# Kernel optimization log

Hardware: AMD Instinct MI355X
Metric: run time of the kernel (lower is better)

Reference implementation:

```python
import jax, jax.numpy as jnp
import numpy as np

# dims: batch, dna_seq_len, protein_emb, decoder_size, ffn hidden, vocab, layers, heads
B, T, P, D, F, V, L, H = 64, 128, 1024, 512, 2048, 4096, 4, 8


def _sinusoid_pe(T, D):
    pos = np.arange(T, dtype=np.float32)[:, None]
    div = np.exp(np.arange(0, D, 2, dtype=np.float32) * (-np.log(10000.0) / D))
    pe = np.zeros((T, D), dtype=np.float32)
    pe[:, 0::2] = np.sin(pos * div)
    pe[:, 1::2] = np.cos(pos * div)
    return jnp.asarray(pe)


def setup_inputs() -> dict:
    key = jax.random.key(0)
    ks = iter(jax.random.split(key, 24))
    n = lambda *shape: jax.random.normal(next(ks), shape, jnp.float32) * 0.02
    return dict(
        protein_embeddings=jax.random.normal(next(ks), (B, P), jnp.float32),
        input_token=jax.random.randint(next(ks), (B,), 0, V),
        proj1_w=n(P, 2 * D), proj1_b=jnp.zeros((2 * D,), jnp.float32),
        proj2_w=n(2 * D, D), proj2_b=jnp.zeros((D,), jnp.float32),
        emb=n(V, D),
        sa_w=n(L, 4, D, D), sa_b=jnp.zeros((L, 4, D), jnp.float32),
        ca_w=n(L, 4, D, D), ca_b=jnp.zeros((L, 4, D), jnp.float32),
        ffn_w1=n(L, D, F), ffn_b1=jnp.zeros((L, F), jnp.float32),
        ffn_w2=n(L, F, D), ffn_b2=jnp.zeros((L, D), jnp.float32),
        ln_g=jnp.ones((L, 3, D), jnp.float32), ln_b=jnp.zeros((L, 3, D), jnp.float32),
        out_w=n(D, V), out_b=jnp.zeros((V,), jnp.float32),
        pe=_sinusoid_pe(T, D),
    )


def _layer_norm(x, g, b, eps=1e-5):
    m = jnp.mean(x, -1, keepdims=True)
    v = jnp.var(x, -1, keepdims=True)
    return (x - m) * jax.lax.rsqrt(v + eps) * g + b


def _forward(protein_embeddings, input_token, proj1_w, proj1_b, proj2_w, proj2_b,
             emb, sa_w, sa_b, ca_w, ca_b, ffn_w1, ffn_b1, ffn_w2, ffn_b2,
             ln_g, ln_b, out_w, out_b, pe):
    dh = D // H
    scale = 1.0 / jnp.sqrt(jnp.float32(dh))
    # protein -> decoder memory: Linear(P, 2D) -> ReLU -> Linear(2D, D),
    # then repeated along seq dim (memory rows are all identical).
    h = jax.nn.relu(protein_embeddings @ proj1_w + proj1_b)
    mem1 = h @ proj2_w + proj2_b                         # [B, D]
    mem = jnp.broadcast_to(mem1[:, None, :], (B, T, D))  # [B, T, D]
    # Cross-attn K/V are constant across decode steps: precompute per layer.
    K = (jnp.einsum('btd,lde->lbte', mem, ca_w[:, 1]) + ca_b[:, 1][:, None, None, :]).reshape(L, B, T, H, dh)
    Vv = (jnp.einsum('btd,lde->lbte', mem, ca_w[:, 2]) + ca_b[:, 2][:, None, None, :]).reshape(L, B, T, H, dh)

    def step(token, t):
        # query length == 1 (the module embeds only the current token each step)
        x = emb[token] + pe[t]                           # [B, D]
        for l in range(L):
            # self-attn over a single key: softmax over one score == 1,
            # so attn output reduces to Wo(Wv x + bv) + bo
            sa = (x @ sa_w[l, 2] + sa_b[l, 2]) @ sa_w[l, 3] + sa_b[l, 3]
            x = _layer_norm(x + sa, ln_g[l, 0], ln_b[l, 0])
            # cross-attention over protein memory
            q = ((x @ ca_w[l, 0] + ca_b[l, 0]) * scale).reshape(B, H, dh)
            s = jnp.einsum('bhe,bthe->bht', q, K[l])
            a = jax.nn.softmax(s, -1)
            o = jnp.einsum('bht,bthe->bhe', a, Vv[l]).reshape(B, D)
            ca = o @ ca_w[l, 3] + ca_b[l, 3]
            x = _layer_norm(x + ca, ln_g[l, 1], ln_b[l, 1])
            # FFN (ReLU, post-LN as in PyTorch default TransformerDecoderLayer)
            f = jax.nn.relu(x @ ffn_w1[l] + ffn_b1[l]) @ ffn_w2[l] + ffn_b2[l]
            x = _layer_norm(x + f, ln_g[l, 2], ln_b[l, 2])
        logits = x @ out_w + out_b                       # [B, V]
        probs = jax.nn.softmax(logits, -1)
        return jnp.argmax(probs, -1), probs

    _, probs_t = jax.lax.scan(step, input_token, jnp.arange(T))
    return jnp.transpose(probs_t, (1, 0, 2))             # [B, T, V]


def reference(protein_embeddings, input_token, proj1_w, proj1_b, proj2_w, proj2_b,
              emb, sa_w, sa_b, ca_w, ca_b, ffn_w1, ffn_b1, ffn_w2, ffn_b2,
              ln_g, ln_b, out_w, out_b, pe):
    return _forward(protein_embeddings, input_token, proj1_w, proj1_b, proj2_w, proj2_b,
                    emb, sa_w, sa_b, ca_w, ca_b, ffn_w1, ffn_b1, ffn_w2, ffn_b2,
                    ln_g, ln_b, out_w, out_b, pe)
```

## Files before the change

### kernel.cpp

```cpp
#include <hip/hip_runtime.h>


#define B 64
#define T 128
#define PP 1024
#define D 512
#define F 2048
#define V 4096
#define XP 20

typedef const float* fp;

static __device__ __forceinline__ float wred(float s){
    #pragma unroll
    for (int o = 32; o > 0; o >>= 1) s += __shfl_xor(s, o, 64);
    return s;
}

__global__ __launch_bounds__(256) void k_setup_mem(
    fp prot, fp p1w, fp p1b, fp p2w, fp p2b,
    fp caw, fp cab, float* ca_out)
{
    __shared__ float xp[PP];
    __shared__ float hr[PP];
    __shared__ float m1[D];
    __shared__ float tv[D];
    int b = blockIdx.x, tid = threadIdx.x;
    for (int i = tid; i < PP; i += 256) xp[i] = prot[b*PP + i];
    __syncthreads();
    for (int c = tid; c < 1024; c += 256){
        float acc = p1b[c];
        for (int k = 0; k < PP; k++) acc = fmaf(xp[k], p1w[k*1024 + c], acc);
        hr[c] = fmaxf(acc, 0.f);
    }
    __syncthreads();
    for (int c = tid; c < D; c += 256){
        float acc = p2b[c];
        for (int k = 0; k < 1024; k++) acc = fmaf(hr[k], p2w[k*D + c], acc);
        m1[c] = acc;
    }
    __syncthreads();
    for (int l = 0; l < 4; l++){
        const float* wv = caw + (size_t)(l*4 + 2)*D*D;
        const float* bv = cab + (l*4 + 2)*D;
        for (int c = tid; c < D; c += 256){
            float acc = bv[c];
            for (int k = 0; k < D; k++) acc = fmaf(m1[k], wv[k*D + c], acc);
            tv[c] = acc;
        }
        __syncthreads();
        const float* wo = caw + (size_t)(l*4 + 3)*D*D;
        const float* bo = cab + (l*4 + 3)*D;
        for (int c = tid; c < D; c += 256){
            float acc = bo[c];
            for (int k = 0; k < D; k++) acc = fmaf(tv[k], wo[k*D + c], acc);
            ca_out[(l*B + b)*D + c] = acc;
        }
        __syncthreads();
    }
}

__global__ __launch_bounds__(256) void k_fold_sa(
    fp saw, fp sab, float* wfold, float* bfold)
{
    int l = blockIdx.x >> 6;
    int kb = blockIdx.x & 63;
    int tid = threadIdx.x;
    const float* Wv = saw + (size_t)(l*4 + 2)*D*D;
    const float* Wo = saw + (size_t)(l*4 + 3)*D*D;
    __shared__ float a[8][D];
    for (int i = tid; i < 8*D; i += 256){
        int r = i >> 9, m = i & 511;
        a[r][m] = Wv[(kb*8 + r)*D + m];
    }
    __syncthreads();
    for (int cc = 0; cc < 2; cc++){
        int c = tid + cc*256;
        float acc[8];
        #pragma unroll
        for (int r = 0; r < 8; r++) acc[r] = 0.f;
        for (int m = 0; m < D; m++){
            float w = Wo[m*D + c];
            #pragma unroll
            for (int r = 0; r < 8; r++) acc[r] = fmaf(a[r][m], w, acc[r]);
        }
        #pragma unroll
        for (int r = 0; r < 8; r++){
            int kg = kb*8 + r;
            wfold[((size_t)l*D + kg)*D + c] = acc[r] + (kg == c ? 1.f : 0.f);
        }
    }
    if (kb == 0){
        const float* bv = sab + (l*4 + 2)*D;
        const float* bo = sab + (l*4 + 3)*D;
        for (int c = tid; c < D; c += 256){
            float acc = bo[c];
            for (int m = 0; m < D; m++) acc = fmaf(bv[m], Wo[m*D + c], acc);
            bfold[l*D + c] = acc;
        }
    }
}


static __device__ void pro_emb(float* xt, const int* tok, fp emb, fp pe,
                               int t, int r0, int d0, int tid)
{
    int lane = tid & 63, wid = tid >> 6;
    for (int i = 0; i < 4; i++){
        int rr = wid*4 + i;
        int tk = tok[r0 + rr];
        const float* er = emb + (size_t)tk*D + d0;
        const float* pr = pe + t*D + d0;
        #pragma unroll
        for (int j = 0; j < 4; j++){
            int d = lane + j*64;
            xt[d*XP + rr] = er[d] + pr[d];
        }
    }
}

static __device__ void pro_ln4(float* xt, const float* u3, fp g, fp bb,
                               int r0, int d0, int tid)
{
    int lane = tid & 63, wid = tid >> 6;
    int jb = d0 >> 6;
    for (int i = 0; i < 4; i++){
        int rr = wid*4 + i, r = r0 + rr;
        float e[8]; float s = 0.f, sq = 0.f;
        #pragma unroll
        for (int j = 0; j < 8; j++){
            int d = lane + j*64;
            float v = u3[r*D + d] + u3[B*D + r*D + d]
                    + u3[2*B*D + r*D + d] + u3[3*B*D + r*D + d];
            e[j] = v; s += v; sq += v*v;
        }
        s = wred(s); sq = wred(sq);
        float mu = s*(1.f/D);
        float rs = rsqrtf(sq*(1.f/D) - mu*mu + 1e-5f);
        #pragma unroll
        for (int j = 0; j < 8; j++){
            int d = lane + j*64;
            if (j >= jb && j < jb + 4)
                xt[(d - d0)*XP + rr] = (e[j]-mu)*rs*g[d] + bb[d];
        }
    }
}

static __device__ void pro_ln2(float* xt, float* zc, const float* u1, const float* ca,
                               fp g0, fp b0, fp g1, fp b1,
                               int r0, int d0, int c0, int tid)
{
    int lane = tid & 63, wid = tid >> 6;
    int jb = d0 >> 6, jc = c0 >> 6;
    for (int i = 0; i < 4; i++){
        int rr = wid*4 + i, r = r0 + rr;
        float e[8]; float s = 0.f, sq = 0.f;
        #pragma unroll
        for (int j = 0; j < 8; j++){
            int d = lane + j*64;
            float v = u1[r*D + d] + u1[B*D + r*D + d];
            e[j] = v; s += v; sq += v*v;
        }
        s = wred(s); sq = wred(sq);
        float mu = s*(1.f/D), rs = rsqrtf(sq*(1.f/D) - mu*mu + 1e-5f);
        s = 0.f; sq = 0.f;
        #pragma unroll
        for (int j = 0; j < 8; j++){
            int d = lane + j*64;
            float v = (e[j]-mu)*rs*g0[d] + b0[d] + ca[r*D + d];
            e[j] = v; s += v; sq += v*v;
        }
        s = wred(s); sq = wred(sq);
        mu = s*(1.f/D); rs = rsqrtf(sq*(1.f/D) - mu*mu + 1e-5f);
        #pragma unroll
        for (int j = 0; j < 8; j++){
            int d = lane + j*64;
            float z = (e[j]-mu)*rs*g1[d] + b1[d];
            if (xt && j >= jb && j < jb + 4) xt[(d - d0)*XP + rr] = z;
            if (zc && j == jc) zc[rr*64 + lane] = z;
        }
    }
}


__global__ __launch_bounds__(256) void k_sa(
    const float* wfold, const float* bfold, const float* u3,
    fp lng, fp lnb, const int* tok, fp emb, fp pe,
    float* u1, int l, int t)
{
    __shared__ float xt[256*XP];
    int bx = blockIdx.x;
    int cb = bx & 7, rbg = (bx >> 3) & 3, ks = bx >> 5;
    int tid = threadIdx.x;
    int r0 = rbg*16, d0 = ks*256;
    if (l == 0) pro_emb(xt, tok, emb, pe, t, r0, d0, tid);
    else        pro_ln4(xt, u3, lng + ((l-1)*3+2)*D, lnb + ((l-1)*3+2)*D, r0, d0, tid);
    __syncthreads();
    int lane = tid & 63, rb = tid >> 6;
    int c = cb*64 + lane;
    const float* W = wfold + (size_t)l*D*D + (size_t)d0*D + c;
    float bias = (ks == 0) ? bfold[l*D + c] : 0.f;
    float a0=bias, a1=bias, a2=bias, a3=bias;
    const float* xc = xt + rb*4;
    #pragma unroll 8
    for (int k = 0; k < 256; k++){
        float w = W[(size_t)k*D];
        float4 xv = *(const float4*)(xc + k*XP);
        a0 = fmaf(xv.x, w, a0); a1 = fmaf(xv.y, w, a1);
        a2 = fmaf(xv.z, w, a2); a3 = fmaf(xv.w, w, a3);
    }
    int r = r0 + rb*4;
    float* o = u1 + ks*B*D;
    o[(r+0)*D + c] = a0; o[(r+1)*D + c] = a1;
    o[(r+2)*D + c] = a2; o[(r+3)*D + c] = a3;
}

__global__ __launch_bounds__(256) void k_ffn1(
    const float* u1, const float* ca, fp lng, fp lnb,
    fp w1, fp b1, float* h, int l)
{
    __shared__ float zt[256*XP];
    int bx = blockIdx.x;
    int cb = bx & 31, rbg = (bx >> 5) & 3, ks = bx >> 7;
    int tid = threadIdx.x;
    int r0 = rbg*16, d0 = ks*256;
    pro_ln2(zt, nullptr, u1, ca + l*B*D,
            lng + l*3*D, lnb + l*3*D, lng + (l*3+1)*D, lnb + (l*3+1)*D,
            r0, d0, 0, tid);
    __syncthreads();
    int lane = tid & 63, rb = tid >> 6;
    int c = cb*64 + lane;
    const float* W = w1 + (size_t)l*D*F + (size_t)d0*F + c;
    float bias = (ks == 0) ? b1[l*F + c] : 0.f;
    float a0=bias, a1=bias, a2=bias, a3=bias;
    const float* xc = zt + rb*4;
    #pragma unroll 8
    for (int k = 0; k < 256; k++){
        float w = W[(size_t)k*F];
        float4 xv = *(const float4*)(xc + k*XP);
        a0 = fmaf(xv.x, w, a0); a1 = fmaf(xv.y, w, a1);
        a2 = fmaf(xv.z, w, a2); a3 = fmaf(xv.w, w, a3);
    }
    int r = r0 + rb*4;
    float* o = h + ks*B*F;
    o[(r+0)*F + c] = a0; o[(r+1)*F + c] = a1;
    o[(r+2)*F + c] = a2; o[(r+3)*F + c] = a3;
}

__global__ __launch_bounds__(256) void k_ffn2(
    const float* u1, const float* ca, fp lng, fp lnb,
    const float* h, fp w2, fp b2, float* u3, int l)
{
    __shared__ float ht[512*XP];
    __shared__ float zc[16*64];
    int bx = blockIdx.x;
    int cb = bx & 7, rbg = (bx >> 3) & 3, kh = bx >> 5;
    int tid = threadIdx.x;
    int r0 = rbg*16, c0 = cb*64;
    if (kh == 0)
        pro_ln2(nullptr, zc, u1, ca + l*B*D,
                lng + l*3*D, lnb + l*3*D, lng + (l*3+1)*D, lnb + (l*3+1)*D,
                r0, 0, c0, tid);
    for (int i = tid; i < 16*512; i += 256){
        int rr = i >> 9, kk = i & 511;
        int gi = (r0+rr)*F + kh*512 + kk;
        ht[kk*XP + rr] = fmaxf(h[gi] + h[B*F + gi], 0.f);
    }
    __syncthreads();
    int lane = tid & 63, rb = tid >> 6;
    int c = c0 + lane;
    const float* W = w2 + (size_t)l*F*D + (size_t)kh*512*D + c;
    float a0, a1, a2, a3;
    if (kh == 0){
        float bb = b2[l*D + c];
        a0 = bb + zc[(rb*4+0)*64 + lane];
        a1 = bb + zc[(rb*4+1)*64 + lane];
        a2 = bb + zc[(rb*4+2)*64 + lane];
        a3 = bb + zc[(rb*4+3)*64 + lane];
    } else { a0=a1=a2=a3=0.f; }
    const float* xc = ht + rb*4;
    #pragma unroll 8
    for (int k = 0; k < 512; k++){
        float w = W[(size_t)k*D];
        float4 xv = *(const float4*)(xc + k*XP);
        a0 = fmaf(xv.x, w, a0); a1 = fmaf(xv.y, w, a1);
        a2 = fmaf(xv.z, w, a2); a3 = fmaf(xv.w, w, a3);
    }
    int r = r0 + rb*4;
    float* o = u3 + kh*B*D;
    o[(r+0)*D + c] = a0; o[(r+1)*D + c] = a1;
    o[(r+2)*D + c] = a2; o[(r+3)*D + c] = a3;
}

__global__ __launch_bounds__(256) void k_logits(
    const float* u3, fp lng, fp lnb, fp outw, fp outb, float* lgt)
{
    __shared__ float xt[256*XP];
    int bx = blockIdx.x;
    int cb = bx & 63, rbg = (bx >> 6) & 3, ks = bx >> 8;
    int tid = threadIdx.x;
    int r0 = rbg*16, d0 = ks*256;
    pro_ln4(xt, u3, lng + 11*D, lnb + 11*D, r0, d0, tid);
    __syncthreads();
    int lane = tid & 63, rb = tid >> 6;
    int c = cb*64 + lane;
    const float* W = outw + (size_t)d0*V + c;
    float bias = (ks == 0) ? outb[c] : 0.f;
    float a0=bias, a1=bias, a2=bias, a3=bias;
    const float* xc = xt + rb*4;
    #pragma unroll 8
    for (int k = 0; k < 256; k++){
        float w = W[(size_t)k*V];
        float4 xv = *(const float4*)(xc + k*XP);
        a0 = fmaf(xv.x, w, a0); a1 = fmaf(xv.y, w, a1);
        a2 = fmaf(xv.z, w, a2); a3 = fmaf(xv.w, w, a3);
    }
    int r = r0 + rb*4;
    float* o = lgt + ks*B*V;
    o[(r+0)*V + c] = a0; o[(r+1)*V + c] = a1;
    o[(r+2)*V + c] = a2; o[(r+3)*V + c] = a3;
}

__global__ __launch_bounds__(256) void k_final(
    const float* lgt, float* out, int* tok, int t)
{
    int b = blockIdx.x, tid = threadIdx.x;
    int lane = tid & 63, wid = tid >> 6;
    __shared__ float sm[4]; __shared__ int si[4]; __shared__ float ss[4];
    const float* l0 = lgt + b*V;
    const float* l1 = lgt + B*V + b*V;
    float m = -3.4e38f; int mi = 0;
    for (int i = tid; i < V; i += 256){
        float v = l0[i] + l1[i];
        if (v > m){ m = v; mi = i; }
    }
    #pragma unroll
    for (int o = 32; o > 0; o >>= 1){
        float om = __shfl_xor(m, o, 64);
        int   oi = __shfl_xor(mi, o, 64);
        if (om > m || (om == m && oi < mi)){ m = om; mi = oi; }
    }
    if (lane == 0){ sm[wid] = m; si[wid] = mi; }
    __syncthreads();
    if (tid == 0){
        #pragma unroll
        for (int w = 1; w < 4; w++)
            if (sm[w] > sm[0] || (sm[w] == sm[0] && si[w] < si[0])){ sm[0]=sm[w]; si[0]=si[w]; }
        tok[b] = si[0];
    }
    __syncthreads();
    m = sm[0];
    float s = 0.f;
    for (int i = tid; i < V; i += 256) s += expf(l0[i] + l1[i] - m);
    s = wred(s);
    if (lane == 0) ss[wid] = s;
    __syncthreads();
    float inv = 1.f / (ss[0] + ss[1] + ss[2] + ss[3]);
    float* orow = out + ((size_t)b*T + t)*V;
    for (int i = tid; i < V; i += 256)
        orow[i] = expf(l0[i] + l1[i] - m) * inv;
}

extern "C" void kernel_launch(void* const* d_in, const int* in_sizes, int n_in,
                              void* d_out, int out_size, void* d_ws, size_t ws_size,
                              hipStream_t stream)
{
    fp prot = (fp)d_in[0];
    const int* itok = (const int*)d_in[1];
    fp p1w=(fp)d_in[2], p1b=(fp)d_in[3], p2w=(fp)d_in[4], p2b=(fp)d_in[5];
    fp emb=(fp)d_in[6], saw=(fp)d_in[7], sab=(fp)d_in[8];
    fp caw=(fp)d_in[9], cab=(fp)d_in[10];
    fp w1=(fp)d_in[11], b1=(fp)d_in[12], w2=(fp)d_in[13], b2=(fp)d_in[14];
    fp lng=(fp)d_in[15], lnb=(fp)d_in[16];
    fp outw=(fp)d_in[17], outb=(fp)d_in[18], pe=(fp)d_in[19];

    char* w = (char*)d_ws;
    float* wfold = (float*)w;  w += (size_t)4*D*D*4;
    float* bfold = (float*)w;  w += 4*D*4;
    float* ca_o  = (float*)w;  w += 4*B*D*4;
    float* u1    = (float*)w;  w += 2*B*D*4;
    float* hbuf  = (float*)w;  w += 2*B*F*4;
    float* u3    = (float*)w;  w += 4*B*D*4;
    float* lgt   = (float*)w;  w += 2*B*V*4;
    int*   tok   = (int*)w;    w += 256;

    float* out = (float*)d_out;

    k_setup_mem<<<64, 256, 0, stream>>>(prot, p1w, p1b, p2w, p2b, caw, cab, ca_o);
    k_fold_sa<<<256, 256, 0, stream>>>(saw, sab, wfold, bfold);

    for (int t = 0; t < T; t++){
        const int* tsrc = (t == 0) ? itok : tok;
        for (int l = 0; l < 4; l++){
            k_sa  <<<64,  256, 0, stream>>>(wfold, bfold, u3, lng, lnb, tsrc, emb, pe, u1, l, t);
            k_ffn1<<<256, 256, 0, stream>>>(u1, ca_o, lng, lnb, w1, b1, hbuf, l);
            k_ffn2<<<128, 256, 0, stream>>>(u1, ca_o, lng, lnb, hbuf, w2, b2, u3, l);
        }
        k_logits<<<512, 256, 0, stream>>>(u3, lng, lnb, outw, outb, lgt);
        k_final <<<64,  256, 0, stream>>>(lgt, out, tok, t);
    }
}
```

Before: 45.07 ms.

## Replace per-step kernel launches with one persistent per-row decode kernel

Replaces the 1,800 small per-step, per-layer kernel launches with a single persistent kernel. It launches one 1024-thread block per batch row, and that block runs all 128 decode steps, the 4 layers, the logits and the softmax/argmax in shared memory. This removes launch overhead and global round-trips of intermediates. In exchange, each of the 64 blocks streams every weight matrix independently from L2/HBM every step, so weight reuse across batch rows is lost. Only 64 CUs are used.

New measurement: 85.22 ms. +89.1%, slower.

```diff
diff --git a/kernel.cpp b/kernel.cpp
--- a/kernel.cpp
+++ b/kernel.cpp
@@ -7,7 +7,6 @@
 #define D 512
 #define F 2048
 #define V 4096
-#define XP 20
 
 typedef const float* fp;
 
@@ -101,264 +100,183 @@
     }
 }
 
-
-static __device__ void pro_emb(float* xt, const int* tok, fp emb, fp pe,
-                               int t, int r0, int d0, int tid)
+__global__ __launch_bounds__(1024) void k_row_decode(
+    const float* wfold, const float* bfold, const float* ca_o,
+    fp lng, fp lnb, const int* itok, fp emb, fp pe,
+    fp w1, fp b1, fp w2, fp b2, fp outw, fp outb, float* out)
 {
-    int lane = tid & 63, wid = tid >> 6;
-    for (int i = 0; i < 4; i++){
-        int rr = wid*4 + i;
-        int tk = tok[r0 + rr];
-        const float* er = emb + (size_t)tk*D + d0;
-        const float* pr = pe + t*D + d0;
-        #pragma unroll
-        for (int j = 0; j < 4; j++){
-            int d = lane + j*64;
-            xt[d*XP + rr] = er[d] + pr[d];
-        }
-    }
-}
-
-static __device__ void pro_ln4(float* xt, const float* u3, fp g, fp bb,
-                               int r0, int d0, int tid)
-{
-    int lane = tid & 63, wid = tid >> 6;
-    int jb = d0 >> 6;
-    for (int i = 0; i < 4; i++){
-        int rr = wid*4 + i, r = r0 + rr;
-        float e[8]; float s = 0.f, sq = 0.f;
-        #pragma unroll
-        for (int j = 0; j < 8; j++){
-            int d = lane + j*64;
-            float v = u3[r*D + d] + u3[B*D + r*D + d]
-                    + u3[2*B*D + r*D + d] + u3[3*B*D + r*D + d];
-            e[j] = v; s += v; sq += v*v;
-        }
-        s = wred(s); sq = wred(sq);
-        float mu = s*(1.f/D);
-        float rs = rsqrtf(sq*(1.f/D) - mu*mu + 1e-5f);
-        #pragma unroll
-        for (int j = 0; j < 8; j++){
-            int d = lane + j*64;
-            if (j >= jb && j < jb + 4)
-                xt[(d - d0)*XP + rr] = (e[j]-mu)*rs*g[d] + bb[d];
-        }
-    }
-}
-
-static __device__ void pro_ln2(float* xt, float* zc, const float* u1, const float* ca,
-                               fp g0, fp b0, fp g1, fp b1,
-                               int r0, int d0, int c0, int tid)
-{
-    int lane = tid & 63, wid = tid >> 6;
-    int jb = d0 >> 6, jc = c0 >> 6;
-    for (int i = 0; i < 4; i++){
-        int rr = wid*4 + i, r = r0 + rr;
-        float e[8]; float s = 0.f, sq = 0.f;
-        #pragma unroll
-        for (int j = 0; j < 8; j++){
-            int d = lane + j*64;
-            float v = u1[r*D + d] + u1[B*D + r*D + d];
-            e[j] = v; s += v; sq += v*v;
-        }
-        s = wred(s); sq = wred(sq);
-        float mu = s*(1.f/D), rs = rsqrtf(sq*(1.f/D) - mu*mu + 1e-5f);
-        s = 0.f; sq = 0.f;
-        #pragma unroll
-        for (int j = 0; j < 8; j++){
-            int d = lane + j*64;
-            float v = (e[j]-mu)*rs*g0[d] + b0[d] + ca[r*D + d];
-            e[j] = v; s += v; sq += v*v;
-        }
-        s = wred(s); sq = wred(sq);
-        mu = s*(1.f/D); rs = rsqrtf(sq*(1.f/D) - mu*mu + 1e-5f);
-        #pragma unroll
-        for (int j = 0; j < 8; j++){
-            int d = lane + j*64;
-            float z = (e[j]-mu)*rs*g1[d] + b1[d];
-            if (xt && j >= jb && j < jb + 4) xt[(d - d0)*XP + rr] = z;
-            if (zc && j == jc) zc[rr*64 + lane] = z;
-        }
-    }
-}
-
-
-__global__ __launch_bounds__(256) void k_sa(
-    const float* wfold, const float* bfold, const float* u3,
-    fp lng, fp lnb, const int* tok, fp emb, fp pe,
-    float* u1, int l, int t)
-{
-    __shared__ float xt[256*XP];
-    int bx = blockIdx.x;
-    int cb = bx & 7, rbg = (bx >> 3) & 3, ks = bx >> 5;
-    int tid = threadIdx.x;
-    int r0 = rbg*16, d0 = ks*256;
-    if (l == 0) pro_emb(xt, tok, emb, pe, t, r0, d0, tid);
-    else        pro_ln4(xt, u3, lng + ((l-1)*3+2)*D, lnb + ((l-1)*3+2)*D, r0, d0, tid);
-    __syncthreads();
-    int lane = tid & 63, rb = tid >> 6;
-    int c = cb*64 + lane;
-    const float* W = wfold + (size_t)l*D*D + (size_t)d0*D + c;
-    float bias = (ks == 0) ? bfold[l*D + c] : 0.f;
-    float a0=bias, a1=bias, a2=bias, a3=bias;
-    const float* xc = xt + rb*4;
-    #pragma unroll 8
-    for (int k = 0; k < 256; k++){
-        float w = W[(size_t)k*D];
-        float4 xv = *(const float4*)(xc + k*XP);
-        a0 = fmaf(xv.x, w, a0); a1 = fmaf(xv.y, w, a1);
-        a2 = fmaf(xv.z, w, a2); a3 = fmaf(xv.w, w, a3);
-    }
-    int r = r0 + rb*4;
-    float* o = u1 + ks*B*D;
-    o[(r+0)*D + c] = a0; o[(r+1)*D + c] = a1;
-    o[(r+2)*D + c] = a2; o[(r+3)*D + c] = a3;
-}
-
-__global__ __launch_bounds__(256) void k_ffn1(
-    const float* u1, const float* ca, fp lng, fp lnb,
-    fp w1, fp b1, float* h, int l)
-{
-    __shared__ float zt[256*XP];
-    int bx = blockIdx.x;
-    int cb = bx & 31, rbg = (bx >> 5) & 3, ks = bx >> 7;
-    int tid = threadIdx.x;
-    int r0 = rbg*16, d0 = ks*256;
-    pro_ln2(zt, nullptr, u1, ca + l*B*D,
-            lng + l*3*D, lnb + l*3*D, lng + (l*3+1)*D, lnb + (l*3+1)*D,
-            r0, d0, 0, tid);
-    __syncthreads();
-    int lane = tid & 63, rb = tid >> 6;
-    int c = cb*64 + lane;
-    const float* W = w1 + (size_t)l*D*F + (size_t)d0*F + c;
-    float bias = (ks == 0) ? b1[l*F + c] : 0.f;
-    float a0=bias, a1=bias, a2=bias, a3=bias;
-    const float* xc = zt + rb*4;
-    #pragma unroll 8
-    for (int k = 0; k < 256; k++){
-        float w = W[(size_t)k*F];
-        float4 xv = *(const float4*)(xc + k*XP);
-        a0 = fmaf(xv.x, w, a0); a1 = fmaf(xv.y, w, a1);
-        a2 = fmaf(xv.z, w, a2); a3 = fmaf(xv.w, w, a3);
-    }
-    int r = r0 + rb*4;
-    float* o = h + ks*B*F;
-    o[(r+0)*F + c] = a0; o[(r+1)*F + c] = a1;
-    o[(r+2)*F + c] = a2; o[(r+3)*F + c] = a3;
-}
-
-__global__ __launch_bounds__(256) void k_ffn2(
-    const float* u1, const float* ca, fp lng, fp lnb,
-    const float* h, fp w2, fp b2, float* u3, int l)
-{
-    __shared__ float ht[512*XP];
-    __shared__ float zc[16*64];
-    int bx = blockIdx.x;
-    int cb = bx & 7, rbg = (bx >> 3) & 3, kh = bx >> 5;
-    int tid = threadIdx.x;
-    int r0 = rbg*16, c0 = cb*64;
-    if (kh == 0)
-        pro_ln2(nullptr, zc, u1, ca + l*B*D,
-                lng + l*3*D, lnb + l*3*D, lng + (l*3+1)*D, lnb + (l*3+1)*D,
-                r0, 0, c0, tid);
-    for (int i = tid; i < 16*512; i += 256){
-        int rr = i >> 9, kk = i & 511;
-        int gi = (r0+rr)*F + kh*512 + kk;
-        ht[kk*XP + rr] = fmaxf(h[gi] + h[B*F + gi], 0.f);
-    }
-    __syncthreads();
-    int lane = tid & 63, rb = tid >> 6;
-    int c = c0 + lane;
-    const float* W = w2 + (size_t)l*F*D + (size_t)kh*512*D + c;
-    float a0, a1, a2, a3;
-    if (kh == 0){
-        float bb = b2[l*D + c];
-        a0 = bb + zc[(rb*4+0)*64 + lane];
-        a1 = bb + zc[(rb*4+1)*64 + lane];
-        a2 = bb + zc[(rb*4+2)*64 + lane];
-        a3 = bb + zc[(rb*4+3)*64 + lane];
-    } else { a0=a1=a2=a3=0.f; }
-    const float* xc = ht + rb*4;
-    #pragma unroll 8
-    for (int k = 0; k < 512; k++){
-        float w = W[(size_t)k*D];
-        float4 xv = *(const float4*)(xc + k*XP);
-        a0 = fmaf(xv.x, w, a0); a1 = fmaf(xv.y, w, a1);
-        a2 = fmaf(xv.z, w, a2); a3 = fmaf(xv.w, w, a3);
-    }
-    int r = r0 + rb*4;
-    float* o = u3 + kh*B*D;
-    o[(r+0)*D + c] = a0; o[(r+1)*D + c] = a1;
-    o[(r+2)*D + c] = a2; o[(r+3)*D + c] = a3;
-}
-
-__global__ __launch_bounds__(256) void k_logits(
-    const float* u3, fp lng, fp lnb, fp outw, fp outb, float* lgt)
-{
-    __shared__ float xt[256*XP];
-    int bx = blockIdx.x;
-    int cb = bx & 63, rbg = (bx >> 6) & 3, ks = bx >> 8;
-    int tid = threadIdx.x;
-    int r0 = rbg*16, d0 = ks*256;
-    pro_ln4(xt, u3, lng + 11*D, lnb + 11*D, r0, d0, tid);
-    __syncthreads();
-    int lane = tid & 63, rb = tid >> 6;
-    int c = cb*64 + lane;
-    const float* W = outw + (size_t)d0*V + c;
-    float bias = (ks == 0) ? outb[c] : 0.f;
-    float a0=bias, a1=bias, a2=bias, a3=bias;
-    const float* xc = xt + rb*4;
-    #pragma unroll 8
-    for (int k = 0; k < 256; k++){
-        float w = W[(size_t)k*V];
-        float4 xv = *(const float4*)(xc + k*XP);
-        a0 = fmaf(xv.x, w, a0); a1 = fmaf(xv.y, w, a1);
-        a2 = fmaf(xv.z, w, a2); a3 = fmaf(xv.w, w, a3);
-    }
-    int r = r0 + rb*4;
-    float* o = lgt + ks*B*V;
-    o[(r+0)*V + c] = a0; o[(r+1)*V + c] = a1;
-    o[(r+2)*V + c] = a2; o[(r+3)*V + c] = a3;
-}
-
-__global__ __launch_bounds__(256) void k_final(
-    const float* lgt, float* out, int* tok, int t)
-{
-    int b = blockIdx.x, tid = threadIdx.x;
-    int lane = tid & 63, wid = tid >> 6;
-    __shared__ float sm[4]; __shared__ int si[4]; __shared__ float ss[4];
-    const float* l0 = lgt + b*V;
-    const float* l1 = lgt + B*V + b*V;
-    float m = -3.4e38f; int mi = 0;
-    for (int i = tid; i < V; i += 256){
-        float v = l0[i] + l1[i];
-        if (v > m){ m = v; mi = i; }
-    }
-    #pragma unroll
-    for (int o = 32; o > 0; o >>= 1){
-        float om = __shfl_xor(m, o, 64);
-        int   oi = __shfl_xor(mi, o, 64);
-        if (om > m || (om == m && oi < mi)){ m = om; mi = oi; }
-    }
-    if (lane == 0){ sm[wid] = m; si[wid] = mi; }
-    __syncthreads();
-    if (tid == 0){
-        #pragma unroll
-        for (int w = 1; w < 4; w++)
-            if (sm[w] > sm[0] || (sm[w] == sm[0] && si[w] < si[0])){ sm[0]=sm[w]; si[0]=si[w]; }
-        tok[b] = si[0];
-    }
-    __syncthreads();
-    m = sm[0];
-    float s = 0.f;
-    for (int i = tid; i < V; i += 256) s += expf(l0[i] + l1[i] - m);
-    s = wred(s);
-    if (lane == 0) ss[wid] = s;
-    __syncthreads();
-    float inv = 1.f / (ss[0] + ss[1] + ss[2] + ss[3]);
-    float* orow = out + ((size_t)b*T + t)*V;
-    for (int i = tid; i < V; i += 256)
-        orow[i] = expf(l0[i] + l1[i] - m) * inv;
+    __shared__ float xv[D];
+    __shared__ float zv[D];
+    __shared__ float hb[F];
+    __shared__ float pr[2048];
+    __shared__ float red[64];
+    __shared__ int  redI[16];
+
+    const int b = blockIdx.x;
+    const int tid = threadIdx.x;
+    const int lane = tid & 63, wave = tid >> 6;
+    const int p = tid & 255, h = tid >> 8;
+    int tok = itok[b];
+
+    for (int t = 0; t < T; t++){
+        if (tid < D) xv[tid] = emb[(size_t)tok*D + tid] + pe[t*D + tid];
+        __syncthreads();
+
+        for (int l = 0; l < 4; l++){
+            {
+                const float* W = wfold + (size_t)l*D*D + (size_t)(h*128)*D + 2*p;
+                const float* xk = xv + h*128;
+                float2 acc = make_float2(0.f, 0.f);
+                #pragma unroll 2
+                for (int k = 0; k < 128; k += 4){
+                    float4 x4 = *(const float4*)(xk + k);
+                    float2 w0 = *(const float2*)(W + (size_t)(k+0)*D);
+                    float2 wA = *(const float2*)(W + (size_t)(k+1)*D);
+                    float2 wB = *(const float2*)(W + (size_t)(k+2)*D);
+                    float2 wC = *(const float2*)(W + (size_t)(k+3)*D);
+                    acc.x = fmaf(x4.x, w0.x, acc.x); acc.y = fmaf(x4.x, w0.y, acc.y);
+                    acc.x = fmaf(x4.y, wA.x, acc.x); acc.y = fmaf(x4.y, wA.y, acc.y);
+                    acc.x = fmaf(x4.z, wB.x, acc.x); acc.y = fmaf(x4.z, wB.y, acc.y);
+                    acc.x = fmaf(x4.w, wC.x, acc.x); acc.y = fmaf(x4.w, wC.y, acc.y);
+                }
+                *(float2*)(pr + h*512 + 2*p) = acc;
+            }
+            __syncthreads();
+            {
+                float u1 = 0.f;
+                if (tid < D)
+                    u1 = pr[tid] + pr[512+tid] + pr[1024+tid] + pr[1536+tid]
+                       + bfold[l*D + tid];
+                float s  = wred(tid < D ? u1 : 0.f);
+                float sq = wred(tid < D ? u1*u1 : 0.f);
+                if (lane == 0){ red[wave] = s; red[16+wave] = sq; }
+                __syncthreads();
+                s = 0.f; sq = 0.f;
+                #pragma unroll
+                for (int w = 0; w < 16; w++){ s += red[w]; sq += red[16+w]; }
+                float mu = s*(1.f/D), rs = rsqrtf(sq*(1.f/D) - mu*mu + 1e-5f);
+                float z0 = 0.f;
+                if (tid < D)
+                    z0 = (u1 - mu)*rs*lng[(l*3)*D + tid] + lnb[(l*3)*D + tid]
+                       + ca_o[((size_t)l*B + b)*D + tid];
+                s  = wred(tid < D ? z0 : 0.f);
+                sq = wred(tid < D ? z0*z0 : 0.f);
+                if (lane == 0){ red[32+wave] = s; red[48+wave] = sq; }
+                __syncthreads();
+                s = 0.f; sq = 0.f;
+                #pragma unroll
+                for (int w = 0; w < 16; w++){ s += red[32+w]; sq += red[48+w]; }
+                mu = s*(1.f/D); rs = rsqrtf(sq*(1.f/D) - mu*mu + 1e-5f);
+                if (tid < D)
+                    zv[tid] = (z0 - mu)*rs*lng[(l*3+1)*D + tid] + lnb[(l*3+1)*D + tid];
+            }
+            __syncthreads();
+            {
+                const float* W = w1 + (size_t)l*D*F + 2*tid;
+                float2 acc = *(const float2*)(b1 + l*F + 2*tid);
+                #pragma unroll 2
+                for (int k = 0; k < D; k += 4){
+                    float4 x4 = *(const float4*)(zv + k);
+                    float2 w0 = *(const float2*)(W + (size_t)(k+0)*F);
+                    float2 wA = *(const float2*)(W + (size_t)(k+1)*F);
+                    float2 wB = *(const float2*)(W + (size_t)(k+2)*F);
+                    float2 wC = *(const float2*)(W + (size_t)(k+3)*F);
+                    acc.x = fmaf(x4.x, w0.x, acc.x); acc.y = fmaf(x4.x, w0.y, acc.y);
+                    acc.x = fmaf(x4.y, wA.x, acc.x); acc.y = fmaf(x4.y, wA.y, acc.y);
+                    acc.x = fmaf(x4.z, wB.x, acc.x); acc.y = fmaf(x4.z, wB.y, acc.y);
+                    acc.x = fmaf(x4.w, wC.x, acc.x); acc.y = fmaf(x4.w, wC.y, acc.y);
+                }
+                *(float2*)(hb + 2*tid) = make_float2(fmaxf(acc.x, 0.f), fmaxf(acc.y, 0.f));
+            }
+            __syncthreads();
+            {
+                const float* W = w2 + (size_t)l*F*D + (size_t)(h*512)*D + 2*p;
+                const float* hk = hb + h*512;
+                float2 acc = make_float2(0.f, 0.f);
+                #pragma unroll 2
+                for (int k = 0; k < 512; k += 4){
+                    float4 x4 = *(const float4*)(hk + k);
+                    float2 w0 = *(const float2*)(W + (size_t)(k+0)*D);
+                    float2 wA = *(const float2*)(W + (size_t)(k+1)*D);
+                    float2 wB = *(const float2*)(W + (size_t)(k+2)*D);
+                    float2 wC = *(const float2*)(W + (size_t)(k+3)*D);
+                    acc.x = fmaf(x4.x, w0.x, acc.x); acc.y = fmaf(x4.x, w0.y, acc.y);
+                    acc.x = fmaf(x4.y, wA.x, acc.x); acc.y = fmaf(x4.y, wA.y, acc.y);
+                    acc.x = fmaf(x4.z, wB.x, acc.x); acc.y = fmaf(x4.z, wB.y, acc.y);
+                    acc.x = fmaf(x4.w, wC.x, acc.x); acc.y = fmaf(x4.w, wC.y, acc.y);
+                }
+                *(float2*)(pr + h*512 + 2*p) = acc;
+            }
+            __syncthreads();
+            {
+                float u3 = 0.f;
+                if (tid < D)
+                    u3 = pr[tid] + pr[512+tid] + pr[1024+tid] + pr[1536+tid]
+                       + b2[l*D + tid] + zv[tid];
+                float s  = wred(tid < D ? u3 : 0.f);
+                float sq = wred(tid < D ? u3*u3 : 0.f);
+                if (lane == 0){ red[wave] = s; red[16+wave] = sq; }
+                __syncthreads();
+                s = 0.f; sq = 0.f;
+                #pragma unroll
+                for (int w = 0; w < 16; w++){ s += red[w]; sq += red[16+w]; }
+                float mu = s*(1.f/D), rs = rsqrtf(sq*(1.f/D) - mu*mu + 1e-5f);
+                if (tid < D)
+                    xv[tid] = (u3 - mu)*rs*lng[(l*3+2)*D + tid] + lnb[(l*3+2)*D + tid];
+            }
+            __syncthreads();
+        }
+
+        float2 accA, accB;
+        {
+            const float* WA = outw + 2*tid;
+            const float* WB = outw + 2048 + 2*tid;
+            accA = *(const float2*)(outb + 2*tid);
+            accB = *(const float2*)(outb + 2048 + 2*tid);
+            #pragma unroll 2
+            for (int k = 0; k < D; k += 2){
+                float2 x2 = *(const float2*)(xv + k);
+                float2 a0 = *(const float2*)(WA + (size_t)(k+0)*V);
+                float2 a1 = *(const float2*)(WA + (size_t)(k+1)*V);
+                float2 c0 = *(const float2*)(WB + (size_t)(k+0)*V);
+                float2 c1 = *(const float2*)(WB + (size_t)(k+1)*V);
+                accA.x = fmaf(x2.x, a0.x, accA.x); accA.y = fmaf(x2.x, a0.y, accA.y);
+                accA.x = fmaf(x2.y, a1.x, accA.x); accA.y = fmaf(x2.y, a1.y, accA.y);
+                accB.x = fmaf(x2.x, c0.x, accB.x); accB.y = fmaf(x2.x, c0.y, accB.y);
+                accB.x = fmaf(x2.y, c1.x, accB.x); accB.y = fmaf(x2.y, c1.y, accB.y);
+            }
+        }
+        int i0 = 2*tid;
+        float m = accA.x; int mi = i0;
+        if (accA.y > m){ m = accA.y; mi = i0 + 1; }
+        if (accB.x > m){ m = accB.x; mi = i0 + 2048; }
+        if (accB.y > m){ m = accB.y; mi = i0 + 2049; }
+        #pragma unroll
+        for (int o = 32; o > 0; o >>= 1){
+            float om = __shfl_xor(m, o, 64);
+            int   oi = __shfl_xor(mi, o, 64);
+            if (om > m || (om == m && oi < mi)){ m = om; mi = oi; }
+        }
+        if (lane == 0){ red[wave] = m; redI[wave] = mi; }
+        __syncthreads();
+        m = red[0]; mi = redI[0];
+        #pragma unroll
+        for (int w = 1; w < 16; w++)
+            if (red[w] > m || (red[w] == m && redI[w] < mi)){ m = red[w]; mi = redI[w]; }
+        float e0 = expf(accA.x - m), e1 = expf(accA.y - m);
+        float e2 = expf(accB.x - m), e3 = expf(accB.y - m);
+        float s = wred(e0 + e1 + e2 + e3);
+        if (lane == 0) red[32 + wave] = s;
+        __syncthreads();
+        s = 0.f;
+        #pragma unroll
+        for (int w = 0; w < 16; w++) s += red[32 + w];
+        float inv = 1.f / s;
+        float* orow = out + ((size_t)b*T + t)*V;
+        *(float2*)(orow + i0)        = make_float2(e0*inv, e1*inv);
+        *(float2*)(orow + i0 + 2048) = make_float2(e2*inv, e3*inv);
+        tok = mi;
+    }
 }
 
 extern "C" void kernel_launch(void* const* d_in, const int* in_sizes, int n_in,
@@ -378,25 +296,12 @@
     float* wfold = (float*)w;  w += (size_t)4*D*D*4;
     float* bfold = (float*)w;  w += 4*D*4;
     float* ca_o  = (float*)w;  w += 4*B*D*4;
-    float* u1    = (float*)w;  w += 2*B*D*4;
-    float* hbuf  = (float*)w;  w += 2*B*F*4;
-    float* u3    = (float*)w;  w += 4*B*D*4;
-    float* lgt   = (float*)w;  w += 2*B*V*4;
-    int*   tok   = (int*)w;    w += 256;
 
     float* out = (float*)d_out;
 
     k_setup_mem<<<64, 256, 0, stream>>>(prot, p1w, p1b, p2w, p2b, caw, cab, ca_o);
     k_fold_sa<<<256, 256, 0, stream>>>(saw, sab, wfold, bfold);
-
-    for (int t = 0; t < T; t++){
-        const int* tsrc = (t == 0) ? itok : tok;
-        for (int l = 0; l < 4; l++){
-            k_sa  <<<64,  256, 0, stream>>>(wfold, bfold, u3, lng, lnb, tsrc, emb, pe, u1, l, t);
-            k_ffn1<<<256, 256, 0, stream>>>(u1, ca_o, lng, lnb, w1, b1, hbuf, l);
-            k_ffn2<<<128, 256, 0, stream>>>(u1, ca_o, lng, lnb, hbuf, w2, b2, u3, l);
-        }
-        k_logits<<<512, 256, 0, stream>>>(u3, lng, lnb, outw, outb, lgt);
-        k_final <<<64,  256, 0, stream>>>(lgt, out, tok, t);
-    }
-}
+    k_row_decode<<<B, 1024, 0, stream>>>(
+        wfold, bfold, ca_o, lng, lnb, itok, emb, pe,
+        w1, b1, w2, b2, outw, outb, out);
+}
```
